# Kernel optimization log

Hardware: AMD Instinct MI355X
Metric: run time of the kernel (lower is better)

The kernel has to match this reference:

```python
import jax, jax.numpy as jnp
import numpy as np

N = 4096
N_STEPS = 50
DT = 0.01
K_SCALE = 0.1
TWO_PI = 6.283185307179586


def setup_inputs() -> dict:
    key = jax.random.key(0)
    k1, k2, k3 = jax.random.split(key, 3)
    # initial phases in [0, 2pi)
    phases = jax.random.uniform(k1, (N,), dtype=jnp.float32) * TWO_PI
    # symmetric learned coupling matrix, as built in __init__
    raw = K_SCALE * jax.random.normal(k2, (N, N), dtype=jnp.float32)
    K = (raw + raw.T) / 2.0
    omegas = jax.random.normal(k3, (N,), dtype=jnp.float32)
    return {"phases": phases, "K": K, "omegas": omegas}


def reference(phases, K, omegas):
    """Euler-integrated Kuramoto dynamics for N_STEPS steps.

    dtheta_i/dt = omega_i + sum_j K[i, j] * sin(theta_j - theta_i)
    """
    dt = jnp.asarray(DT, dtype=phases.dtype)

    def step(theta, _):
        # diff[i, j] = theta_j - theta_i
        diff = theta[None, :] - theta[:, None]          # (n, n)
        coupling = jnp.sum(K * jnp.sin(diff), axis=1)   # (n,)
        theta_new = theta + dt * (omegas + coupling)
        return theta_new, None

    final, _ = jax.lax.scan(step, phases, None, length=N_STEPS)
    return final
```

## Files before the change

kernel.cpp:

```cpp
#include <hip/hip_runtime.h>
#include <math.h>


#define NOSC 4096
#define NSTEPS 50
#define DTF 0.01f

__device__ __forceinline__ float bf_lo(unsigned int w) {
  return __uint_as_float(w << 16);
}
__device__ __forceinline__ float bf_hi(unsigned int w) {
  return __uint_as_float(w & 0xFFFF0000u);
}

__global__ __launch_bounds__(256) void k_convert(
    const float4* __restrict__ K4, ushort4* __restrict__ Kb,
    const float* __restrict__ phases, float* __restrict__ theta,
    float* __restrict__ s0, float* __restrict__ c0) {
  if (blockIdx.x < 16) {
    const int i = blockIdx.x * 256 + threadIdx.x;
    const float t = phases[i];
    theta[i] = t;
    s0[i] = sinf(t);
    c0[i] = cosf(t);
  }
  const int n4 = NOSC * NOSC / 4;
  for (int i = blockIdx.x * 256 + threadIdx.x; i < n4;
       i += gridDim.x * 256) {
    const float4 f = K4[i];
    ushort4 o;
    unsigned int b;
    b = __float_as_uint(f.x); b += 0x7FFFu + ((b >> 16) & 1u); o.x = (unsigned short)(b >> 16);
    b = __float_as_uint(f.y); b += 0x7FFFu + ((b >> 16) & 1u); o.y = (unsigned short)(b >> 16);
    b = __float_as_uint(f.z); b += 0x7FFFu + ((b >> 16) & 1u); o.z = (unsigned short)(b >> 16);
    b = __float_as_uint(f.w); b += 0x7FFFu + ((b >> 16) & 1u); o.w = (unsigned short)(b >> 16);
    Kb[i] = o;
  }
}

template <bool BF16K>
__global__ __launch_bounds__(256, 2) void k_step(
    const void* __restrict__ Kp, const float* __restrict__ omegas,
    float* __restrict__ theta,
    const float* __restrict__ s_in, const float* __restrict__ c_in,
    float* __restrict__ s_out, float* __restrict__ c_out) {
  __shared__ float s_lds[NOSC];
  __shared__ float c_lds[NOSC];
  const int tid = threadIdx.x;
  const int lane = tid & 63;
  const int wv = tid >> 6;
  const int base = ((blockIdx.x & 7) << 9) + ((blockIdx.x >> 3) << 3);
  const int r0 = base + 2 * wv;
  const int r1 = r0 + 1;

  float4* sl4 = reinterpret_cast<float4*>(s_lds);
  float4* cl4 = reinterpret_cast<float4*>(c_lds);
  const float4* sg4 = reinterpret_cast<const float4*>(s_in);
  const float4* cg4 = reinterpret_cast<const float4*>(c_in);
  #pragma unroll
  for (int i = 0; i < 4; ++i) {
    const int idx = i * 256 + tid;
    sl4[idx] = sg4[idx];
    cl4[idx] = cg4[idx];
  }
  __syncthreads();

  float aS0 = 0.f, aC0 = 0.f, aS1 = 0.f, aC1 = 0.f;
  if (BF16K) {
    const unsigned short* Kb = reinterpret_cast<const unsigned short*>(Kp);
    const uint4* Ka = reinterpret_cast<const uint4*>(Kb + (size_t)r0 * NOSC);
    const uint4* Kc = reinterpret_cast<const uint4*>(Kb + (size_t)r1 * NOSC);
    #pragma unroll
    for (int ch = 0; ch < 8; ++ch) {
      const int idx = (ch << 6) + lane;
      const uint4 ka = Ka[idx];
      const uint4 kb = Kc[idx];
      const float4 sv0 = sl4[2 * idx], sv1 = sl4[2 * idx + 1];
      const float4 cv0 = cl4[2 * idx], cv1 = cl4[2 * idx + 1];
      float k;
      k = bf_lo(ka.x); aS0 = fmaf(k, sv0.x, aS0); aC0 = fmaf(k, cv0.x, aC0);
      k = bf_hi(ka.x); aS0 = fmaf(k, sv0.y, aS0); aC0 = fmaf(k, cv0.y, aC0);
      k = bf_lo(ka.y); aS0 = fmaf(k, sv0.z, aS0); aC0 = fmaf(k, cv0.z, aC0);
      k = bf_hi(ka.y); aS0 = fmaf(k, sv0.w, aS0); aC0 = fmaf(k, cv0.w, aC0);
      k = bf_lo(ka.z); aS0 = fmaf(k, sv1.x, aS0); aC0 = fmaf(k, cv1.x, aC0);
      k = bf_hi(ka.z); aS0 = fmaf(k, sv1.y, aS0); aC0 = fmaf(k, cv1.y, aC0);
      k = bf_lo(ka.w); aS0 = fmaf(k, sv1.z, aS0); aC0 = fmaf(k, cv1.z, aC0);
      k = bf_hi(ka.w); aS0 = fmaf(k, sv1.w, aS0); aC0 = fmaf(k, cv1.w, aC0);
      k = bf_lo(kb.x); aS1 = fmaf(k, sv0.x, aS1); aC1 = fmaf(k, cv0.x, aC1);
      k = bf_hi(kb.x); aS1 = fmaf(k, sv0.y, aS1); aC1 = fmaf(k, cv0.y, aC1);
      k = bf_lo(kb.y); aS1 = fmaf(k, sv0.z, aS1); aC1 = fmaf(k, cv0.z, aC1);
      k = bf_hi(kb.y); aS1 = fmaf(k, sv0.w, aS1); aC1 = fmaf(k, cv0.w, aC1);
      k = bf_lo(kb.z); aS1 = fmaf(k, sv1.x, aS1); aC1 = fmaf(k, cv1.x, aC1);
      k = bf_hi(kb.z); aS1 = fmaf(k, sv1.y, aS1); aC1 = fmaf(k, cv1.y, aC1);
      k = bf_lo(kb.w); aS1 = fmaf(k, sv1.z, aS1); aC1 = fmaf(k, cv1.z, aC1);
      k = bf_hi(kb.w); aS1 = fmaf(k, sv1.w, aS1); aC1 = fmaf(k, cv1.w, aC1);
    }
  } else {
    const float* Kf = reinterpret_cast<const float*>(Kp);
    const float4* Ka = reinterpret_cast<const float4*>(Kf + (size_t)r0 * NOSC);
    const float4* Kc = reinterpret_cast<const float4*>(Kf + (size_t)r1 * NOSC);
    #pragma unroll
    for (int ch = 0; ch < 16; ++ch) {
      const int idx = (ch << 6) + lane;
      const float4 k0 = Ka[idx], k1 = Kc[idx];
      const float4 sv = sl4[idx], cv = cl4[idx];
      aS0 = fmaf(k0.x, sv.x, aS0); aS0 = fmaf(k0.y, sv.y, aS0);
      aS0 = fmaf(k0.z, sv.z, aS0); aS0 = fmaf(k0.w, sv.w, aS0);
      aC0 = fmaf(k0.x, cv.x, aC0); aC0 = fmaf(k0.y, cv.y, aC0);
      aC0 = fmaf(k0.z, cv.z, aC0); aC0 = fmaf(k0.w, cv.w, aC0);
      aS1 = fmaf(k1.x, sv.x, aS1); aS1 = fmaf(k1.y, sv.y, aS1);
      aS1 = fmaf(k1.z, sv.z, aS1); aS1 = fmaf(k1.w, sv.w, aS1);
      aC1 = fmaf(k1.x, cv.x, aC1); aC1 = fmaf(k1.y, cv.y, aC1);
      aC1 = fmaf(k1.z, cv.z, aC1); aC1 = fmaf(k1.w, cv.w, aC1);
    }
  }

  #pragma unroll
  for (int off = 32; off > 0; off >>= 1) {
    aS0 += __shfl_xor(aS0, off); aC0 += __shfl_xor(aC0, off);
    aS1 += __shfl_xor(aS1, off); aC1 += __shfl_xor(aC1, off);
  }
  const int myRow = (lane == 0) ? r0 : ((lane == 1) ? r1 : -1);
  if (myRow >= 0) {
    const float accS = (lane == 0) ? aS0 : aS1;
    const float accC = (lane == 0) ? aC0 : aC1;
    const float si = s_lds[myRow];
    const float ci = c_lds[myRow];
    const float tn = theta[myRow] + DTF * (omegas[myRow] + ci * accS - si * accC);
    theta[myRow] = tn;
    s_out[myRow] = sinf(tn);
    c_out[myRow] = cosf(tn);
  }
}

__global__ __launch_bounds__(256) void k_init_fb(
    const float* __restrict__ phases, float* __restrict__ theta,
    float* __restrict__ svec, float* __restrict__ cvec) {
  const int i = blockIdx.x * 256 + threadIdx.x;
  const float t = phases[i];
  theta[i] = t;
  svec[i] = sinf(t);
  cvec[i] = cosf(t);
}

extern "C" void kernel_launch(void* const* d_in, const int* in_sizes, int n_in,
                              void* d_out, int out_size, void* d_ws, size_t ws_size,
                              hipStream_t stream) {
  const float* phases = (const float*)d_in[0];
  const float* Kmat   = (const float*)d_in[1];
  const float* omegas = (const float*)d_in[2];
  float* out = (float*)d_out;

  float* ws = (float*)d_ws;
  float* theta = ws + 0 * NOSC;
  float* sb[2] = {ws + 1 * NOSC, ws + 3 * NOSC};
  float* cb[2] = {ws + 2 * NOSC, ws + 4 * NOSC};

  const size_t headBytes = (size_t)5 * NOSC * sizeof(float);
  const size_t kbOff = (headBytes + 255) & ~(size_t)255;
  const size_t kbBytes = (size_t)NOSC * NOSC * 2;
  const bool useBf16 = (ws_size >= kbOff + kbBytes);
  unsigned short* Kb = (unsigned short*)((char*)d_ws + kbOff);

  if (useBf16) {
    k_convert<<<2048, 256, 0, stream>>>((const float4*)Kmat, (ushort4*)Kb,
                                        phases, theta, sb[0], cb[0]);
    for (int t = 0; t < NSTEPS; ++t) {
      k_step<true><<<512, 256, 0, stream>>>(
          (const void*)Kb, omegas, theta, sb[t & 1], cb[t & 1],
          sb[(t + 1) & 1], cb[(t + 1) & 1]);
    }
  } else {
    k_init_fb<<<NOSC / 256, 256, 0, stream>>>(phases, theta, sb[0], cb[0]);
    for (int t = 0; t < NSTEPS; ++t) {
      k_step<false><<<512, 256, 0, stream>>>(
          (const void*)Kmat, omegas, theta, sb[t & 1], cb[t & 1],
          sb[(t + 1) & 1], cb[(t + 1) & 1]);
    }
  }
  hipMemcpyAsync(out, theta, NOSC * sizeof(float), hipMemcpyDeviceToDevice,
                 stream);
}
```

Measured before the change: 307.6 us.

## Replace per-step launches with persistent kernel holding bf16 K rows in LDS

Fuses the conversion and all 50 Euler steps into one persistent kernel of 256 blocks. Each block converts its 16 rows of K to bf16 and keeps them in LDS, so K is read from HBM only once. Steps are synchronised through a global atomic counter barrier. sin/cos of the updated phases are advanced with a small-angle Taylor rotation instead of calling sinf/cosf. This removes 50 kernel launches and the repeated reads of K, but it depends on all blocks being co-resident, has a spin-timeout escape that could break correctness, and lets rotation error accumulate.

Result: slower. 917.0 us (+198.1%).

```diff
diff --git a/kernel.cpp b/kernel.cpp
--- a/kernel.cpp
+++ b/kernel.cpp
@@ -5,6 +5,13 @@
 #define NOSC 4096
 #define NSTEPS 50
 #define DTF 0.01f
+#define NBLK 256
+#define NTHR 512
+#define ROWS 16
+#define CPT 8
+#define KLDSB (ROWS * NOSC * 2)
+#define SCRB  (8 * 32 * 8 * 4)
+#define LDSB  (KLDSB + SCRB)
 
 __device__ __forceinline__ float bf_lo(unsigned int w) {
   return __uint_as_float(w << 16);
@@ -13,124 +20,142 @@
   return __uint_as_float(w & 0xFFFF0000u);
 }
 
-__global__ __launch_bounds__(256) void k_convert(
-    const float4* __restrict__ K4, ushort4* __restrict__ Kb,
-    const float* __restrict__ phases, float* __restrict__ theta,
-    float* __restrict__ s0, float* __restrict__ c0) {
-  if (blockIdx.x < 16) {
-    const int i = blockIdx.x * 256 + threadIdx.x;
-    const float t = phases[i];
-    theta[i] = t;
-    s0[i] = sinf(t);
-    c0[i] = cosf(t);
-  }
-  const int n4 = NOSC * NOSC / 4;
-  for (int i = blockIdx.x * 256 + threadIdx.x; i < n4;
-       i += gridDim.x * 256) {
-    const float4 f = K4[i];
-    ushort4 o;
-    unsigned int b;
-    b = __float_as_uint(f.x); b += 0x7FFFu + ((b >> 16) & 1u); o.x = (unsigned short)(b >> 16);
-    b = __float_as_uint(f.y); b += 0x7FFFu + ((b >> 16) & 1u); o.y = (unsigned short)(b >> 16);
-    b = __float_as_uint(f.z); b += 0x7FFFu + ((b >> 16) & 1u); o.z = (unsigned short)(b >> 16);
-    b = __float_as_uint(f.w); b += 0x7FFFu + ((b >> 16) & 1u); o.w = (unsigned short)(b >> 16);
-    Kb[i] = o;
-  }
-}
-
-template <bool BF16K>
-__global__ __launch_bounds__(256, 2) void k_step(
-    const void* __restrict__ Kp, const float* __restrict__ omegas,
-    float* __restrict__ theta,
-    const float* __restrict__ s_in, const float* __restrict__ c_in,
-    float* __restrict__ s_out, float* __restrict__ c_out) {
-  __shared__ float s_lds[NOSC];
-  __shared__ float c_lds[NOSC];
+extern "C" __global__ __launch_bounds__(NTHR, 2) void k_persist(
+    const float* __restrict__ phases, const float* __restrict__ Kmat,
+    const float* __restrict__ omegas, float* __restrict__ out,
+    float2* __restrict__ scG, unsigned long long* __restrict__ cnt) {
+  extern __shared__ unsigned char lds_raw[];
+  unsigned short* K_lds = (unsigned short*)lds_raw;
+  float* scr = (float*)(lds_raw + KLDSB);
+
   const int tid = threadIdx.x;
   const int lane = tid & 63;
   const int wv = tid >> 6;
-  const int base = ((blockIdx.x & 7) << 9) + ((blockIdx.x >> 3) << 3);
-  const int r0 = base + 2 * wv;
-  const int r1 = r0 + 1;
-
-  float4* sl4 = reinterpret_cast<float4*>(s_lds);
-  float4* cl4 = reinterpret_cast<float4*>(c_lds);
-  const float4* sg4 = reinterpret_cast<const float4*>(s_in);
-  const float4* cg4 = reinterpret_cast<const float4*>(c_in);
+  const int b = blockIdx.x;
+
+  const float4* src =
+      reinterpret_cast<const float4*>(Kmat + (size_t)b * ROWS * NOSC);
+  #pragma unroll 4
+  for (int q = 0; q < 32; ++q) {
+    const int idx = q * NTHR + tid;
+    const float4 f = src[idx];
+    ushort4 o;
+    unsigned int u;
+    u = __float_as_uint(f.x); u += 0x7FFFu + ((u >> 16) & 1u); o.x = (unsigned short)(u >> 16);
+    u = __float_as_uint(f.y); u += 0x7FFFu + ((u >> 16) & 1u); o.y = (unsigned short)(u >> 16);
+    u = __float_as_uint(f.z); u += 0x7FFFu + ((u >> 16) & 1u); o.z = (unsigned short)(u >> 16);
+    u = __float_as_uint(f.w); u += 0x7FFFu + ((u >> 16) & 1u); o.w = (unsigned short)(u >> 16);
+    *reinterpret_cast<ushort4*>(&K_lds[idx * 4]) = o;
+  }
+
+  float sreg[CPT], creg[CPT];
   #pragma unroll
-  for (int i = 0; i < 4; ++i) {
-    const int idx = i * 256 + tid;
-    sl4[idx] = sg4[idx];
-    cl4[idx] = cg4[idx];
+  for (int i = 0; i < CPT; ++i) {
+    const float ph = phases[CPT * tid + i];
+    sreg[i] = sinf(ph);
+    creg[i] = cosf(ph);
+  }
+  float thR = 0.f, omR = 0.f, sR = 0.f, cR = 0.f;
+  if (tid < ROWS) {
+    const int gi = b * ROWS + tid;
+    thR = phases[gi];
+    omR = omegas[gi];
+    sR = sinf(thR);
+    cR = cosf(thR);
   }
   __syncthreads();
 
-  float aS0 = 0.f, aC0 = 0.f, aS1 = 0.f, aC1 = 0.f;
-  if (BF16K) {
-    const unsigned short* Kb = reinterpret_cast<const unsigned short*>(Kp);
-    const uint4* Ka = reinterpret_cast<const uint4*>(Kb + (size_t)r0 * NOSC);
-    const uint4* Kc = reinterpret_cast<const uint4*>(Kb + (size_t)r1 * NOSC);
-    #pragma unroll
-    for (int ch = 0; ch < 8; ++ch) {
-      const int idx = (ch << 6) + lane;
-      const uint4 ka = Ka[idx];
-      const uint4 kb = Kc[idx];
-      const float4 sv0 = sl4[2 * idx], sv1 = sl4[2 * idx + 1];
-      const float4 cv0 = cl4[2 * idx], cv1 = cl4[2 * idx + 1];
+  for (int step = 0; step < NSTEPS; ++step) {
+    float pS[ROWS], pC[ROWS];
+    #pragma unroll
+    for (int r = 0; r < ROWS; ++r) { pS[r] = 0.f; pC[r] = 0.f; }
+    #pragma unroll
+    for (int r = 0; r < ROWS; ++r) {
+      const uint4 kw =
+          *reinterpret_cast<const uint4*>(&K_lds[r * NOSC + CPT * tid]);
       float k;
-      k = bf_lo(ka.x); aS0 = fmaf(k, sv0.x, aS0); aC0 = fmaf(k, cv0.x, aC0);
-      k = bf_hi(ka.x); aS0 = fmaf(k, sv0.y, aS0); aC0 = fmaf(k, cv0.y, aC0);
-      k = bf_lo(ka.y); aS0 = fmaf(k, sv0.z, aS0); aC0 = fmaf(k, cv0.z, aC0);
-      k = bf_hi(ka.y); aS0 = fmaf(k, sv0.w, aS0); aC0 = fmaf(k, cv0.w, aC0);
-      k = bf_lo(ka.z); aS0 = fmaf(k, sv1.x, aS0); aC0 = fmaf(k, cv1.x, aC0);
-      k = bf_hi(ka.z); aS0 = fmaf(k, sv1.y, aS0); aC0 = fmaf(k, cv1.y, aC0);
-      k = bf_lo(ka.w); aS0 = fmaf(k, sv1.z, aS0); aC0 = fmaf(k, cv1.z, aC0);
-      k = bf_hi(ka.w); aS0 = fmaf(k, sv1.w, aS0); aC0 = fmaf(k, cv1.w, aC0);
-      k = bf_lo(kb.x); aS1 = fmaf(k, sv0.x, aS1); aC1 = fmaf(k, cv0.x, aC1);
-      k = bf_hi(kb.x); aS1 = fmaf(k, sv0.y, aS1); aC1 = fmaf(k, cv0.y, aC1);
-      k = bf_lo(kb.y); aS1 = fmaf(k, sv0.z, aS1); aC1 = fmaf(k, cv0.z, aC1);
-      k = bf_hi(kb.y); aS1 = fmaf(k, sv0.w, aS1); aC1 = fmaf(k, cv0.w, aC1);
-      k = bf_lo(kb.z); aS1 = fmaf(k, sv1.x, aS1); aC1 = fmaf(k, cv1.x, aC1);
-      k = bf_hi(kb.z); aS1 = fmaf(k, sv1.y, aS1); aC1 = fmaf(k, cv1.y, aC1);
-      k = bf_lo(kb.w); aS1 = fmaf(k, sv1.z, aS1); aC1 = fmaf(k, cv1.z, aC1);
-      k = bf_hi(kb.w); aS1 = fmaf(k, sv1.w, aS1); aC1 = fmaf(k, cv1.w, aC1);
-    }
-  } else {
-    const float* Kf = reinterpret_cast<const float*>(Kp);
-    const float4* Ka = reinterpret_cast<const float4*>(Kf + (size_t)r0 * NOSC);
-    const float4* Kc = reinterpret_cast<const float4*>(Kf + (size_t)r1 * NOSC);
-    #pragma unroll
-    for (int ch = 0; ch < 16; ++ch) {
-      const int idx = (ch << 6) + lane;
-      const float4 k0 = Ka[idx], k1 = Kc[idx];
-      const float4 sv = sl4[idx], cv = cl4[idx];
-      aS0 = fmaf(k0.x, sv.x, aS0); aS0 = fmaf(k0.y, sv.y, aS0);
-      aS0 = fmaf(k0.z, sv.z, aS0); aS0 = fmaf(k0.w, sv.w, aS0);
-      aC0 = fmaf(k0.x, cv.x, aC0); aC0 = fmaf(k0.y, cv.y, aC0);
-      aC0 = fmaf(k0.z, cv.z, aC0); aC0 = fmaf(k0.w, cv.w, aC0);
-      aS1 = fmaf(k1.x, sv.x, aS1); aS1 = fmaf(k1.y, sv.y, aS1);
-      aS1 = fmaf(k1.z, sv.z, aS1); aS1 = fmaf(k1.w, sv.w, aS1);
-      aC1 = fmaf(k1.x, cv.x, aC1); aC1 = fmaf(k1.y, cv.y, aC1);
-      aC1 = fmaf(k1.z, cv.z, aC1); aC1 = fmaf(k1.w, cv.w, aC1);
-    }
-  }
-
-  #pragma unroll
-  for (int off = 32; off > 0; off >>= 1) {
-    aS0 += __shfl_xor(aS0, off); aC0 += __shfl_xor(aC0, off);
-    aS1 += __shfl_xor(aS1, off); aC1 += __shfl_xor(aC1, off);
-  }
-  const int myRow = (lane == 0) ? r0 : ((lane == 1) ? r1 : -1);
-  if (myRow >= 0) {
-    const float accS = (lane == 0) ? aS0 : aS1;
-    const float accC = (lane == 0) ? aC0 : aC1;
-    const float si = s_lds[myRow];
-    const float ci = c_lds[myRow];
-    const float tn = theta[myRow] + DTF * (omegas[myRow] + ci * accS - si * accC);
-    theta[myRow] = tn;
-    s_out[myRow] = sinf(tn);
-    c_out[myRow] = cosf(tn);
-  }
+      k = bf_lo(kw.x); pS[r] = fmaf(k, sreg[0], pS[r]); pC[r] = fmaf(k, creg[0], pC[r]);
+      k = bf_hi(kw.x); pS[r] = fmaf(k, sreg[1], pS[r]); pC[r] = fmaf(k, creg[1], pC[r]);
+      k = bf_lo(kw.y); pS[r] = fmaf(k, sreg[2], pS[r]); pC[r] = fmaf(k, creg[2], pC[r]);
+      k = bf_hi(kw.y); pS[r] = fmaf(k, sreg[3], pS[r]); pC[r] = fmaf(k, creg[3], pC[r]);
+      k = bf_lo(kw.z); pS[r] = fmaf(k, sreg[4], pS[r]); pC[r] = fmaf(k, creg[4], pC[r]);
+      k = bf_hi(kw.z); pS[r] = fmaf(k, sreg[5], pS[r]); pC[r] = fmaf(k, creg[5], pC[r]);
+      k = bf_lo(kw.w); pS[r] = fmaf(k, sreg[6], pS[r]); pC[r] = fmaf(k, creg[6], pC[r]);
+      k = bf_hi(kw.w); pS[r] = fmaf(k, sreg[7], pS[r]); pC[r] = fmaf(k, creg[7], pC[r]);
+    }
+
+    #pragma unroll
+    for (int off = 1; off <= 4; off <<= 1) {
+      #pragma unroll
+      for (int r = 0; r < ROWS; ++r) {
+        pS[r] += __shfl_xor(pS[r], off);
+        pC[r] += __shfl_xor(pC[r], off);
+      }
+    }
+    if ((lane & 7) == 0) {
+      const int g = lane >> 3;
+      float* base = scr + wv * 256 + g;
+      #pragma unroll
+      for (int r = 0; r < ROWS; ++r) {
+        base[(2 * r) * 8] = pS[r];
+        base[(2 * r + 1) * 8] = pC[r];
+      }
+    }
+    __syncthreads();
+
+    if (tid < ROWS) {
+      float S = 0.f, C = 0.f;
+      #pragma unroll
+      for (int w = 0; w < 8; ++w) {
+        const float4* p4 =
+            reinterpret_cast<const float4*>(scr + w * 256 + 16 * tid);
+        const float4 a = p4[0], bq = p4[1];
+        const float4 c4 = p4[2], d4 = p4[3];
+        S += (a.x + a.y) + (a.z + a.w) + (bq.x + bq.y) + (bq.z + bq.w);
+        C += (c4.x + c4.y) + (c4.z + c4.w) + (d4.x + d4.y) + (d4.z + d4.w);
+      }
+      const float delta = DTF * (omR + cR * S - sR * C);
+      thR += delta;
+      const float d2 = delta * delta;
+      const float sd = delta * fmaf(d2, fmaf(d2, 1.f / 120.f, -1.f / 6.f), 1.f);
+      const float cd = fmaf(d2, fmaf(d2, 1.f / 24.f, -0.5f), 1.f);
+      const float ns = fmaf(sR, cd, cR * sd);
+      const float nc = fmaf(cR, cd, -sR * sd);
+      sR = ns;
+      cR = nc;
+      const unsigned long long bits =
+          ((unsigned long long)__float_as_uint(nc) << 32) | __float_as_uint(ns);
+      __hip_atomic_store((unsigned long long*)&scG[b * ROWS + tid], bits,
+                         __ATOMIC_RELAXED, __HIP_MEMORY_SCOPE_AGENT);
+    }
+    if (step == NSTEPS - 1) break;
+
+    __syncthreads();
+    if (tid == 0) {
+      __threadfence();
+      __hip_atomic_fetch_add(cnt, 1ull, __ATOMIC_RELEASE,
+                             __HIP_MEMORY_SCOPE_AGENT);
+      const unsigned long long tgt = (unsigned long long)(step + 1) * NBLK;
+      unsigned int spins = 0;
+      while (__hip_atomic_load(cnt, __ATOMIC_ACQUIRE,
+                               __HIP_MEMORY_SCOPE_AGENT) < tgt) {
+        __builtin_amdgcn_s_sleep(2);
+        if (++spins > (1u << 20)) break;
+      }
+    }
+    __syncthreads();
+
+    #pragma unroll
+    for (int i = 0; i < CPT; ++i) {
+      const unsigned long long bits = __hip_atomic_load(
+          (const unsigned long long*)&scG[CPT * tid + i], __ATOMIC_RELAXED,
+          __HIP_MEMORY_SCOPE_AGENT);
+      sreg[i] = __uint_as_float((unsigned int)bits);
+      creg[i] = __uint_as_float((unsigned int)(bits >> 32));
+    }
+  }
+
+  if (tid < ROWS) out[b * ROWS + tid] = thR;
 }
 
 __global__ __launch_bounds__(256) void k_init_fb(
@@ -143,6 +168,50 @@
   cvec[i] = cosf(t);
 }
 
+__global__ __launch_bounds__(256, 2) void k_step_full(
+    const float* __restrict__ Kf, const float* __restrict__ omegas,
+    float* __restrict__ theta,
+    const float* __restrict__ s_in, const float* __restrict__ c_in,
+    float* __restrict__ s_out, float* __restrict__ c_out) {
+  const int lane = threadIdx.x & 63;
+  const int wave = threadIdx.x >> 6;
+  const int row0 = (blockIdx.x << 3) + (wave << 1);
+  const int row1 = row0 + 1;
+  const float4* s4 = reinterpret_cast<const float4*>(s_in);
+  const float4* c4 = reinterpret_cast<const float4*>(c_in);
+  const float4* K40 = reinterpret_cast<const float4*>(Kf + (size_t)row0 * NOSC);
+  const float4* K41 = reinterpret_cast<const float4*>(Kf + (size_t)row1 * NOSC);
+  float aS0 = 0.f, aC0 = 0.f, aS1 = 0.f, aC1 = 0.f;
+  #pragma unroll
+  for (int ch = 0; ch < 16; ++ch) {
+    const int idx = (ch << 6) + lane;
+    float4 k0 = K40[idx], k1 = K41[idx], sv = s4[idx], cv = c4[idx];
+    aS0 = fmaf(k0.x, sv.x, aS0); aS0 = fmaf(k0.y, sv.y, aS0);
+    aS0 = fmaf(k0.z, sv.z, aS0); aS0 = fmaf(k0.w, sv.w, aS0);
+    aC0 = fmaf(k0.x, cv.x, aC0); aC0 = fmaf(k0.y, cv.y, aC0);
+    aC0 = fmaf(k0.z, cv.z, aC0); aC0 = fmaf(k0.w, cv.w, aC0);
+    aS1 = fmaf(k1.x, sv.x, aS1); aS1 = fmaf(k1.y, sv.y, aS1);
+    aS1 = fmaf(k1.z, sv.z, aS1); aS1 = fmaf(k1.w, sv.w, aS1);
+    aC1 = fmaf(k1.x, cv.x, aC1); aC1 = fmaf(k1.y, cv.y, aC1);
+    aC1 = fmaf(k1.z, cv.z, aC1); aC1 = fmaf(k1.w, cv.w, aC1);
+  }
+  #pragma unroll
+  for (int off = 32; off > 0; off >>= 1) {
+    aS0 += __shfl_xor(aS0, off); aC0 += __shfl_xor(aC0, off);
+    aS1 += __shfl_xor(aS1, off); aC1 += __shfl_xor(aC1, off);
+  }
+  const int myRow = (lane == 0) ? row0 : ((lane == 1) ? row1 : -1);
+  if (myRow >= 0) {
+    const float accS = (lane == 0) ? aS0 : aS1;
+    const float accC = (lane == 0) ? aC0 : aC1;
+    const float tn = theta[myRow] +
+        DTF * (omegas[myRow] + c_in[myRow] * accS - s_in[myRow] * accC);
+    theta[myRow] = tn;
+    s_out[myRow] = sinf(tn);
+    c_out[myRow] = cosf(tn);
+  }
+}
+
 extern "C" void kernel_launch(void* const* d_in, const int* in_sizes, int n_in,
                               void* d_out, int out_size, void* d_ws, size_t ws_size,
                               hipStream_t stream) {
@@ -151,33 +220,32 @@
   const float* omegas = (const float*)d_in[2];
   float* out = (float*)d_out;
 
-  float* ws = (float*)d_ws;
-  float* theta = ws + 0 * NOSC;
-  float* sb[2] = {ws + 1 * NOSC, ws + 3 * NOSC};
-  float* cb[2] = {ws + 2 * NOSC, ws + 4 * NOSC};
-
-  const size_t headBytes = (size_t)5 * NOSC * sizeof(float);
-  const size_t kbOff = (headBytes + 255) & ~(size_t)255;
-  const size_t kbBytes = (size_t)NOSC * NOSC * 2;
-  const bool useBf16 = (ws_size >= kbOff + kbBytes);
-  unsigned short* Kb = (unsigned short*)((char*)d_ws + kbOff);
-
-  if (useBf16) {
-    k_convert<<<2048, 256, 0, stream>>>((const float4*)Kmat, (ushort4*)Kb,
-                                        phases, theta, sb[0], cb[0]);
-    for (int t = 0; t < NSTEPS; ++t) {
-      k_step<true><<<512, 256, 0, stream>>>(
-          (const void*)Kb, omegas, theta, sb[t & 1], cb[t & 1],
-          sb[(t + 1) & 1], cb[(t + 1) & 1]);
-    }
+  float2* scG = (float2*)d_ws;
+  unsigned long long* cnt =
+      (unsigned long long*)((char*)d_ws + (size_t)NOSC * 8);
+
+  bool ok = (ws_size >= (size_t)NOSC * 8 + 64 + 6 * NOSC * 4);
+  if (ok) {
+    ok = (hipFuncSetAttribute((const void*)k_persist,
+                              hipFuncAttributeMaxDynamicSharedMemorySize,
+                              LDSB) == hipSuccess);
+  }
+
+  if (ok) {
+    hipMemsetAsync(cnt, 0, sizeof(unsigned long long), stream);
+    k_persist<<<NBLK, NTHR, LDSB, stream>>>(phases, Kmat, omegas, out, scG, cnt);
   } else {
+    float* base = (float*)((char*)d_ws + (size_t)NOSC * 8 + 64);
+    float* theta = base;
+    float* sb[2] = {base + 1 * NOSC, base + 3 * NOSC};
+    float* cb[2] = {base + 2 * NOSC, base + 4 * NOSC};
     k_init_fb<<<NOSC / 256, 256, 0, stream>>>(phases, theta, sb[0], cb[0]);
     for (int t = 0; t < NSTEPS; ++t) {
-      k_step<false><<<512, 256, 0, stream>>>(
-          (const void*)Kmat, omegas, theta, sb[t & 1], cb[t & 1],
+      k_step_full<<<NOSC / 8, 256, 0, stream>>>(
+          Kmat, omegas, theta, sb[t & 1], cb[t & 1],
           sb[(t + 1) & 1], cb[(t + 1) & 1]);
     }
-  }
-  hipMemcpyAsync(out, theta, NOSC * sizeof(float), hipMemcpyDeviceToDevice,
-                 stream);
-}
+    hipMemcpyAsync(out, theta, NOSC * sizeof(float), hipMemcpyDeviceToDevice,
+                   stream);
+  }
+}
```
